# Kernel optimization log

Hardware: AMD Instinct MI355X
Metric: run time of the kernel (lower is better)

Reference implementation:

```python
import jax, jax.numpy as jnp
import numpy as np

# static config (matches init_kwargs / source constants)
B, S, CCH, NF, T = 64, 50, 3, 129, 29   # batch, seq, channels, freq bins (nfft/2+1), frames
M_FB = 32                                # filterbank size M in F1
D = 16                                   # latents -> SPD matrix size
M_OFF = D * (D - 1) // 2                 # strictly-lower Cholesky entries
HID = D + M_OFF                          # ODE state size
ODE_U = 256                              # n_units
NCLS = 5
K_EULER, DT = 4, 0.25                    # fixed-step Euler ODE solve per interval
BN_EPS = 1e-5


def lin_tri_filter(nfilt=M_FB, nfft=256, samplerate=100):
    # faithful port of FilterbankShape.lin_tri_filter_shape
    highfreq = samplerate / 2
    hz = np.linspace(0, highfreq, nfilt + 2)
    b = np.floor((nfft + 1) * hz / samplerate)
    fb = np.zeros([nfilt, nfft // 2 + 1])
    for j in range(nfilt):
        for i in range(int(b[j]), int(b[j + 1])):
            fb[j, i] = (i - b[j]) / (b[j + 1] - b[j])
        for i in range(int(b[j + 1]), int(b[j + 2])):
            fb[j, i] = (b[j + 2] - i) / (b[j + 2] - b[j + 1])
    return fb.T.astype(np.float32)  # (129, 32)


def setup_inputs() -> dict:
    key = jax.random.key(0)
    ks = jax.random.split(key, 32)
    f32 = jnp.float32
    CIN = CCH * M_FB  # 96

    def unif(k, shape, bound):
        return jax.random.uniform(k, shape, f32, -bound, bound)

    sd = 1.0 / np.sqrt(D)
    so = 1.0 / np.sqrt(M_OFF)
    cb1 = 1.0 / np.sqrt(CIN * 5)
    cb2 = 1.0 / np.sqrt(CIN * 5)
    lb = lambda fan_in: 1.0 / np.sqrt(fan_in)

    inp = {
        "x": jax.random.normal(ks[0], (B, S, CCH, NF, T), f32),
        "fw": jax.nn.sigmoid(jax.random.normal(ks[1], (NF, M_FB), f32)),
        "s_tri": jnp.asarray(lin_tri_filter()),
        "conv1_w": unif(ks[2], (CIN, CIN, 5), cb1),
        "conv1_b": unif(ks[3], (CIN,), cb1),
        "bn1_g": jnp.ones((CIN,), f32),
        "bn1_b": jnp.zeros((CIN,), f32),
        "conv2_w": unif(ks[4], (D, CIN, 5), cb2),
        "conv2_b": unif(ks[5], (D,), cb2),
        "bn2_g": jnp.ones((D,), f32),
        "bn2_b": jnp.zeros((D,), f32),
        "wx_d": unif(ks[6], (D, 3 * D), sd),
        "wh_d": unif(ks[7], (D, 3 * D), sd),
        "bias_d": unif(ks[8], (3 * D,), sd),
        "wx_o": unif(ks[9], (M_OFF, 3 * M_OFF), so),
        "wh_o": unif(ks[10], (M_OFF, 3 * M_OFF), so),
        "bias_o": unif(ks[11], (3 * M_OFF,), so),
        "ode_w0": unif(ks[12], (HID, ODE_U), lb(HID)),
        "ode_b0": unif(ks[13], (ODE_U,), lb(HID)),
        "ode_w1": unif(ks[14], (ODE_U, ODE_U), lb(ODE_U)),
        "ode_b1": unif(ks[15], (ODE_U,), lb(ODE_U)),
        "ode_w2": unif(ks[16], (ODE_U, ODE_U), lb(ODE_U)),
        "ode_b2": unif(ks[17], (ODE_U,), lb(ODE_U)),
        "ode_w3": unif(ks[18], (ODE_U, HID), lb(ODE_U)),
        "ode_b3": unif(ks[19], (HID,), lb(ODE_U)),
        "cls_w": unif(ks[20], (HID, NCLS), lb(HID)),
        "cls_b": unif(ks[21], (NCLS,), lb(HID)),
    }
    return inp


def _forward(x, fw, s_tri, conv1_w, conv1_b, bn1_g, bn1_b, conv2_w, conv2_b,
             bn2_g, bn2_b, wx_d, wh_d, bias_d, wx_o, wh_o, bias_o,
             ode_w0, ode_b0, ode_w1, ode_b1, ode_w2, ode_b2, ode_w3, ode_b3,
             cls_w, cls_b):
    b, s = x.shape[:2]
    # --- filter_bank: (b,s,C,F,T) x (F,M) -> (b,s,C*M,T) ---
    xf = jnp.einsum('bscft,fm->bscmt', x, fw * s_tri)
    h = xf.reshape(b * s, CCH * M_FB, T)
    dn = ('NCH', 'OIH', 'NCH')

    def conv_bn_lrelu(h, w, bias, g, be):
        h = jax.lax.conv_general_dilated(h, w, (1,), 'VALID', dimension_numbers=dn)
        h = h + bias[None, :, None]
        mu = h.mean((0, 2), keepdims=True)           # BatchNorm1d (train-mode stats)
        var = h.var((0, 2), keepdims=True)
        h = (h - mu) / jnp.sqrt(var + BN_EPS) * g[None, :, None] + be[None, :, None]
        return jnp.where(h >= 0, h, 0.01 * h)        # LeakyReLU

    h = conv_bn_lrelu(h, conv1_w, conv1_b, bn1_g, bn1_b)   # (bs, 96, 25)
    h = conv_bn_lrelu(h, conv2_w, conv2_b, bn2_g, bn2_b)   # (bs, D, 21)
    feats = h.transpose(0, 2, 1)                           # (bs, t, D)

    def oas(X):  # OAS-shrunk covariance, X: (n, d)
        n, d = X.shape
        xm = X - X.mean(0)
        emp = xm.T @ xm / (n - 1)
        mu = jnp.trace(emp) / d
        alpha = jnp.mean(emp ** 2)
        num = alpha + mu ** 2
        den = (n + 1.0) * (alpha - mu ** 2 / d)
        shr = jnp.where(den == 0, 1.0, jnp.minimum(num / den, 1.0))
        return (1.0 - shr) * emp + shr * mu * jnp.eye(d, dtype=X.dtype)

    covs = jax.vmap(oas)(feats)                            # (bs, D, D)
    L = jnp.linalg.cholesky(covs).reshape(b, s, D, D)
    ir, ic = np.tril_indices(D, -1)
    x_d = jnp.diagonal(L, axis1=-2, axis2=-1)              # (b,s,D) positive
    x_o = L[..., ir, ic]                                   # (b,s,M_OFF)

    def ode_net(hh):  # odefunc: Lin, [Tanh,Lin]*2, Tanh, Lin
        hh = hh @ ode_w0 + ode_b0
        hh = jnp.tanh(hh) @ ode_w1 + ode_b1
        hh = jnp.tanh(hh) @ ode_w2 + ode_b2
        return jnp.tanh(hh) @ ode_w3 + ode_b3

    abs_bd = jnp.abs(bias_d)

    def step(carry, xt):
        hd, ho = carry
        xd, xo = xt
        # ODE evolution of hidden state in Cholesky chart (log-diag || off-diag)
        hc = jnp.concatenate([jnp.log(hd), ho], -1)
        for _ in range(K_EULER):
            hc = hc + DT * ode_net(hc)
        hd = jnp.exp(hc[:, :D])
        ho = hc[:, D:]
        # diag RGRU cell (PosLinear + softplus; log/exp products simplify)
        gx = xd @ jnp.abs(wx_d)
        gh = hd @ jnp.abs(wh_d)
        ixr, ixi, ixn = jnp.split(gx, 3, 1)
        hhr, hhi, hhn = jnp.split(gh, 3, 1)
        br, bi, bn = jnp.split(abs_bd, 3)
        r = jax.nn.sigmoid(br * ixr * hhr)
        z = jax.nn.sigmoid(bi * ixi * hhi)
        ng = jax.nn.softplus(bn * ixn * r * hhn)
        hd = hd ** z * ng ** (1.0 - z)   # geodesic GRU update on positive diag
        # off-diag RGRU cell (standard Euclidean GRU)
        gx = xo @ wx_o
        gh = ho @ wh_o
        ixr, ixi, ixn = jnp.split(gx, 3, 1)
        hhr, hhi, hhn = jnp.split(gh, 3, 1)
        br2, bi2, bn2 = jnp.split(bias_o, 3)
        r = jax.nn.sigmoid(ixr + hhr + br2)
        z = jax.nn.sigmoid(ixi + hhi + bi2)
        ng = jnp.tanh(ixn + r * hhn + bn2)
        ho = ng + z * (ho - ng)
        return (hd, ho), None

    hd0 = jnp.ones((b, D), x.dtype)
    ho0 = jnp.zeros((b, M_OFF), x.dtype)
    (hd, ho), _ = jax.lax.scan(step, (hd0, ho0),
                               (x_d.transpose(1, 0, 2), x_o.transpose(1, 0, 2)))
    feat = jnp.concatenate([jnp.log(hd), ho], -1)
    return feat @ cls_w + cls_b  # (b, NCLS)


def reference(x, fw, s_tri, conv1_w, conv1_b, bn1_g, bn1_b, conv2_w, conv2_b,
              bn2_g, bn2_b, wx_d, wh_d, bias_d, wx_o, wh_o, bias_o,
              ode_w0, ode_b0, ode_w1, ode_b1, ode_w2, ode_b2, ode_w3, ode_b3,
              cls_w, cls_b):
    return _forward(x, fw, s_tri, conv1_w, conv1_b, bn1_g, bn1_b, conv2_w,
                    conv2_b, bn2_g, bn2_b, wx_d, wh_d, bias_d, wx_o, wh_o,
                    bias_o, ode_w0, ode_b0, ode_w1, ode_b1, ode_w2, ode_b2,
                    ode_w3, ode_b3, cls_w, cls_b)
```

## Files before the change

### kernel.cpp

```cpp
#include <hip/hip_runtime.h>
#include <math.h>


#define BB 64
#define NIMG 3200

typedef _Float16 f16;
typedef _Float16 f16x8 __attribute__((ext_vector_type(8)));
typedef float f32x4 __attribute__((ext_vector_type(4)));

#define HS 164
#define GS 516

__device__ __forceinline__ float fsigm(float x) {
  return __fdividef(1.f, 1.f + __expf(-x));
}
__device__ __forceinline__ float ftanh(float x) {
  return 1.f - __fdividef(2.f, __expf(2.f * x) + 1.f);
}

#define OFF_W0  0
#define OFF_W1  20480
#define OFF_W2  53248
#define OFF_W3  86016
#define OFF_GRZ 104448
#define OFF_GNX 135168
#define OFF_GNH 143360
#define PK2_TOT 151552

__global__ __launch_bounds__(256) void k1_fb(const float* __restrict__ x,
                                             const float* __restrict__ fw,
                                             const float* __restrict__ st,
                                             float* __restrict__ h1) {
  __shared__ __align__(16) float ws[129 * 32];
  __shared__ __align__(16) float xs[129 * 32];
  const int tid = threadIdx.x;
  const int n = blockIdx.x;
  const float* xp = x + (size_t)n * 11223;

  for (int i = tid; i < 4128; i += 256) ws[i] = fw[i] * st[i];

  float acc[4][4];
#pragma unroll
  for (int i = 0; i < 4; ++i)
#pragma unroll
    for (int j = 0; j < 4; ++j) acc[i][j] = 0.f;

  const int c = tid / 64;
  const int rem = tid % 64;
  const int m0 = (rem / 8) * 4;
  const int t0 = (rem % 8) * 4;

  for (int fc = 0; fc < 3; ++fc) {
    __syncthreads();
    for (int i = tid; i < 3741; i += 256) {
      int cc = i / 1247;
      int r = i - cc * 1247;
      int f = r / 29;
      int t = r - f * 29;
      xs[(cc * 43 + f) * 32 + t] = xp[cc * 3741 + (fc * 43 + f) * 29 + t];
    }
    for (int i = tid; i < 129; i += 256) {
      xs[i * 32 + 29] = 0.f; xs[i * 32 + 30] = 0.f; xs[i * 32 + 31] = 0.f;
    }
    __syncthreads();
    if (tid < 192) {
      const float* xb = xs + (c * 43) * 32 + t0;
      const float* wb = ws + (fc * 43) * 32 + m0;
      for (int f = 0; f < 43; ++f) {
        float4 xv = *(const float4*)(xb + f * 32);
        float4 wv = *(const float4*)(wb + f * 32);
        float xa[4] = {xv.x, xv.y, xv.z, xv.w};
        float wa[4] = {wv.x, wv.y, wv.z, wv.w};
#pragma unroll
        for (int i = 0; i < 4; ++i)
#pragma unroll
          for (int j = 0; j < 4; ++j) acc[i][j] += wa[i] * xa[j];
      }
    }
  }
  if (tid < 192) {
    const int nt = (t0 == 28) ? 1 : 4;
    for (int i = 0; i < 4; ++i)
      for (int j = 0; j < nt; ++j)
        h1[(size_t)n * 2784 + (size_t)(c * 32 + m0 + i) * 29 + (t0 + j)] = acc[i][j];
  }
}

__global__ __launch_bounds__(256) void k2_conv1(const float* __restrict__ h1,
                                                const float* __restrict__ w,
                                                const float* __restrict__ bias,
                                                float* __restrict__ h2,
                                                float* __restrict__ part1) {
  __shared__ __align__(16) float ins[2 * 96 * 32];
  __shared__ __align__(16) float wls[96 * 81];
  const int tid = threadIdx.x;
  const int wg = blockIdx.x;

  for (int i = tid; i < 2 * 2784; i += 256) {
    int img = i / 2784;
    int e = i - img * 2784;
    int ci = e / 29;
    int t = e - ci * 29;
    ins[img * 3072 + ci * 32 + t] = h1[(size_t)(wg * 2 + img) * 2784 + e];
  }

  const int img = tid / 96;
  const int co = tid - img * 96;
  float acc[25];
#pragma unroll
  for (int t = 0; t < 25; ++t) acc[t] = 0.f;

  for (int cc = 0; cc < 6; ++cc) {
    __syncthreads();
    for (int i = tid; i < 7680; i += 256) {
      int cw = i / 80;
      int r = i - cw * 80;
      wls[cw * 81 + r] = w[cw * 480 + cc * 80 + r];
    }
    __syncthreads();
    if (tid < 192) {
      for (int ci = 0; ci < 16; ++ci) {
        float xv[29];
#pragma unroll
        for (int j = 0; j < 29; ++j) xv[j] = ins[img * 3072 + (cc * 16 + ci) * 32 + j];
        float wv[5];
#pragma unroll
        for (int d = 0; d < 5; ++d) wv[d] = wls[co * 81 + ci * 5 + d];
#pragma unroll
        for (int t = 0; t < 25; ++t) {
          float s = acc[t];
#pragma unroll
          for (int d = 0; d < 5; ++d) s += xv[t + d] * wv[d];
          acc[t] = s;
        }
      }
    }
  }
  if (tid < 192) {
    const int n = wg * 2 + img;
    const float bval = bias[co];
    float s1 = 0.f, s2 = 0.f;
    for (int t = 0; t < 25; ++t) {
      float v = acc[t] + bval;
      h2[(size_t)n * 2400 + co * 25 + t] = v;
      s1 += v;
      s2 += v * v;
    }
    part1[((size_t)n * 96 + co) * 2 + 0] = s1;
    part1[((size_t)n * 96 + co) * 2 + 1] = s2;
  }
}

__global__ __launch_bounds__(256) void k3_bn1(const float* __restrict__ part,
                                              const float* __restrict__ gg,
                                              const float* __restrict__ be,
                                              float* __restrict__ ab) {
  __shared__ double sd[256], sq[256];
  const int c = blockIdx.x;
  const int t = threadIdx.x;
  double s = 0.0, q = 0.0;
  for (int n = t; n < NIMG; n += 256) {
    s += (double)part[((size_t)n * 96 + c) * 2 + 0];
    q += (double)part[((size_t)n * 96 + c) * 2 + 1];
  }
  sd[t] = s; sq[t] = q;
  __syncthreads();
  for (int off = 128; off > 0; off >>= 1) {
    if (t < off) { sd[t] += sd[t + off]; sq[t] += sq[t + off]; }
    __syncthreads();
  }
  if (t == 0) {
    double mu = sd[0] / 80000.0;
    double var = sq[0] / 80000.0 - mu * mu;
    float A = (float)((double)gg[c] / sqrt(var + 1e-5));
    ab[c * 2 + 0] = A;
    ab[c * 2 + 1] = (float)((double)be[c] - mu * (double)A);
  }
}

__global__ __launch_bounds__(256) void k5_bn2(const float* __restrict__ part,
                                              const float* __restrict__ gg,
                                              const float* __restrict__ be,
                                              float* __restrict__ ab) {
  __shared__ double sd[256], sq[256];
  const int c = blockIdx.x;
  const int t = threadIdx.x;
  double s = 0.0, q = 0.0;
  for (int n = t; n < 800; n += 256) {
    s += (double)part[((size_t)n * 16 + c) * 2 + 0];
    q += (double)part[((size_t)n * 16 + c) * 2 + 1];
  }
  sd[t] = s; sq[t] = q;
  __syncthreads();
  for (int off = 128; off > 0; off >>= 1) {
    if (t < off) { sd[t] += sd[t + off]; sq[t] += sq[t + off]; }
    __syncthreads();
  }
  if (t == 0) {
    double mu = sd[0] / 67200.0;
    double var = sq[0] / 67200.0 - mu * mu;
    float A = (float)((double)gg[c] / sqrt(var + 1e-5));
    ab[c * 2 + 0] = A;
    ab[c * 2 + 1] = (float)((double)be[c] - mu * (double)A);
  }
}

__global__ __launch_bounds__(256) void k4_conv2(const float* __restrict__ h2,
                                                const float* __restrict__ w,
                                                const float* __restrict__ bias,
                                                const float* __restrict__ bn1,
                                                float* __restrict__ h3,
                                                float* __restrict__ part2) {
  __shared__ __align__(16) float ins[4 * 96 * 26];
  __shared__ __align__(16) float wls[16 * 241];
  __shared__ float A1s[96], B1s[96];
  __shared__ float red[16 * 16 * 2];
  const int tid = threadIdx.x;
  const int wg = blockIdx.x;

  if (tid < 96) {
    A1s[tid] = bn1[tid * 2 + 0];
    B1s[tid] = bn1[tid * 2 + 1];
  }
  __syncthreads();
  for (int i = tid; i < 9600; i += 256) {
    int img = i / 2400;
    int e = i - img * 2400;
    int ci = e / 25;
    int t = e - ci * 25;
    float v = h2[(size_t)(wg * 4 + img) * 2400 + e];
    v = A1s[ci] * v + B1s[ci];
    v = (v >= 0.f) ? v : 0.01f * v;
    ins[img * 2496 + ci * 26 + t] = v;
  }
  for (int i = tid; i < 4 * 96; i += 256) ins[(i / 96) * 2496 + (i % 96) * 26 + 25] = 0.f;

  const int img = tid >> 6;
  const int co = (tid >> 2) & 15;
  const int tg = tid & 3;
  const int t0s[4] = {0, 6, 11, 16};
  const int t0 = t0s[tg];
  const int tl = (tg == 0) ? 6 : 5;
  float acc[6] = {0.f, 0.f, 0.f, 0.f, 0.f, 0.f};

  for (int cc = 0; cc < 2; ++cc) {
    __syncthreads();
    for (int i = tid; i < 3840; i += 256) {
      int cw = i / 240;
      int r = i - cw * 240;
      wls[cw * 241 + r] = w[cw * 480 + cc * 240 + r];
    }
    __syncthreads();
    for (int ci = 0; ci < 48; ++ci) {
      float xv[10];
#pragma unroll
      for (int j = 0; j < 10; ++j) xv[j] = ins[img * 2496 + (cc * 48 + ci) * 26 + t0 + j];
      float wv[5];
#pragma unroll
      for (int d = 0; d < 5; ++d) wv[d] = wls[co * 241 + ci * 5 + d];
#pragma unroll
      for (int t = 0; t < 6; ++t) {
        float s = acc[t];
#pragma unroll
        for (int d = 0; d < 5; ++d) s += xv[t + d] * wv[d];
        acc[t] = s;
      }
    }
  }
  const float bval = bias[co];
  float s1 = 0.f, s2 = 0.f;
  const int n = wg * 4 + img;
  for (int t = 0; t < 6; ++t) {
    if (t < tl) {
      float v = acc[t] + bval;
      h3[(size_t)n * 336 + co * 21 + t0 + t] = v;
      s1 += v;
      s2 += v * v;
    }
  }
  red[(co * 16 + img * 4 + tg) * 2 + 0] = s1;
  red[(co * 16 + img * 4 + tg) * 2 + 1] = s2;
  __syncthreads();
  if (tid < 16) {
    float s = 0.f, q = 0.f;
    for (int k = 0; k < 16; ++k) {
      s += red[(tid * 16 + k) * 2 + 0];
      q += red[(tid * 16 + k) * 2 + 1];
    }
    part2[((size_t)wg * 16 + tid) * 2 + 0] = s;
    part2[((size_t)wg * 16 + tid) * 2 + 1] = q;
  }
}

__global__ __launch_bounds__(256) void k6_oas(const float* __restrict__ h3,
                                              const float* __restrict__ bn2,
                                              float* __restrict__ xd,
                                              float* __restrict__ xo) {
  __shared__ float X[4][21 * 17 + 3];
  __shared__ float A[4][16 * 17];
  __shared__ float mcol[4][16];
  const int tid = threadIdx.x;
  const int wid = tid >> 6;
  const int lane = tid & 63;
  const int n = blockIdx.x * 4 + wid;
  const float* hp = h3 + (size_t)n * 336;

  for (int e = lane; e < 336; e += 64) {
    int c = e / 21;
    int t = e - c * 21;
    float v = hp[e];
    v = bn2[c * 2 + 0] * v + bn2[c * 2 + 1];
    v = (v >= 0.f) ? v : 0.01f * v;
    X[wid][t * 17 + c] = v;
  }
  __syncthreads();
  if (lane < 16) {
    float s = 0.f;
    for (int t = 0; t < 21; ++t) s += X[wid][t * 17 + lane];
    mcol[wid][lane] = s * (1.f / 21.f);
  }
  __syncthreads();
  for (int e = lane; e < 336; e += 64) {
    int t = e / 16;
    int c = e - t * 16;
    X[wid][t * 17 + c] -= mcol[wid][c];
  }
  __syncthreads();

  float tr_p = 0.f, al_p = 0.f;
  float ent[3];
  int ei[3], ej[3], ne = 0;
  for (int e = lane; e < 136; e += 64) {
    int i = 0, e2 = e;
    while (e2 >= 16 - i) { e2 -= 16 - i; i++; }
    int j = i + e2;
    float s = 0.f;
    for (int t = 0; t < 21; ++t) s += X[wid][t * 17 + i] * X[wid][t * 17 + j];
    s *= (1.f / 20.f);
    ent[ne] = s; ei[ne] = i; ej[ne] = j; ne++;
    if (i == j) tr_p += s;
    al_p += s * s * ((i == j) ? 1.f : 2.f);
  }
  for (int m = 1; m < 64; m <<= 1) {
    tr_p += __shfl_xor(tr_p, m);
    al_p += __shfl_xor(al_p, m);
  }
  const float mu = tr_p * (1.f / 16.f);
  const float alpha = al_p * (1.f / 256.f);
  const float num = alpha + mu * mu;
  const float den = 22.f * (alpha - mu * mu * (1.f / 16.f));
  const float shr = (den == 0.f) ? 1.f : fminf(num / den, 1.f);
  for (int q = 0; q < ne; ++q) {
    float c = (1.f - shr) * ent[q] + ((ei[q] == ej[q]) ? shr * mu : 0.f);
    A[wid][ei[q] * 17 + ej[q]] = c;
    A[wid][ej[q] * 17 + ei[q]] = c;
  }
  __syncthreads();

  for (int k = 0; k < 16; ++k) {
    float akk = A[wid][k * 17 + k];
    __syncthreads();
    float d = sqrtf(akk);
    float rd = 1.f / d;
    if (lane == k) A[wid][k * 17 + k] = d;
    if (lane > k && lane < 16) A[wid][lane * 17 + k] *= rd;
    __syncthreads();
    if (lane > k && lane < 16) {
      float Lik = A[wid][lane * 17 + k];
      for (int j = k + 1; j <= lane; ++j) A[wid][lane * 17 + j] -= Lik * A[wid][j * 17 + k];
    }
    __syncthreads();
  }
  if (lane < 16) xd[(size_t)n * 16 + lane] = A[wid][lane * 17 + lane];
  for (int p = lane; p < 120; p += 64) {
    int i = 1, p2 = p;
    while (p2 >= i) { p2 -= i; i++; }
    xo[(size_t)n * 120 + p] = A[wid][i * 17 + p2];
  }
}

__global__ __launch_bounds__(256) void k0_pack(const float* __restrict__ w0,
                                               const float* __restrict__ w1,
                                               const float* __restrict__ w2,
                                               const float* __restrict__ w3,
                                               const float* __restrict__ wxo,
                                               const float* __restrict__ who,
                                               uint32_t* __restrict__ dst) {
  int i = blockIdx.x * 256 + threadIdx.x;
  if (i >= PK2_TOT) return;
  int j = i, kind, NT;
  if (j < OFF_W1)       { kind = 0; NT = 16; }
  else if (j < OFF_W2)  { kind = 1; NT = 16; j -= OFF_W1; }
  else if (j < OFF_W3)  { kind = 2; NT = 16; j -= OFF_W2; }
  else if (j < OFF_GRZ) { kind = 3; NT = 9;  j -= OFF_W3; }
  else if (j < OFF_GNX) { kind = 4; NT = 15; j -= OFF_GRZ; }
  else if (j < OFF_GNH) { kind = 5; NT = 8;  j -= OFF_GNX; }
  else                  { kind = 6; NT = 8;  j -= OFF_GNH; }
  const int tile = j >> 8;
  const int rem = j & 255;
  const int l = rem >> 2;
  const int wd = rem & 3;
  const int t = tile / NT;
  const int nt = tile - t * NT;
  const int col = nt * 16 + (l & 15);
  const int kk = t * 32 + 8 * (l >> 4) + 2 * wd;

  float v[2];
#pragma unroll
  for (int q = 0; q < 2; ++q) {
    const int k = kk + q;
    float s = 0.f;
    if (kind == 0)      { if (k < 136) s = w0[k * 256 + col]; }
    else if (kind == 1) { s = w1[k * 256 + col]; }
    else if (kind == 2) { s = w2[k * 256 + col]; }
    else if (kind == 3) { if (col < 136) s = w3[k * 136 + col]; }
    else if (kind == 4) {
      if (k < 120) s = wxo[k * 360 + col];
      else if (k >= 128 && k < 248) s = who[(k - 128) * 360 + col];
    } else if (kind == 5) { if (k < 120 && col < 120) s = wxo[k * 360 + 240 + col]; }
    else                  { if (k < 120 && col < 120) s = who[k * 360 + 240 + col]; }
    v[q] = s;
  }
  union { f16 h[2]; uint32_t u; } cv;
  cv.h[0] = (f16)v[0];
  cv.h[1] = (f16)v[1];
  dst[i] = cv.u;
}

__device__ __forceinline__ uint4 aread_lin(const f16* X, int t, int l) {
  return ((const uint4*)X)[t * 64 + l];
}
__device__ __forceinline__ void xwrite_frag(f16* X, int row, int col, float v) {
  const int slot = row + 16 * ((col >> 3) & 3);
  const int byte = (((col >> 5) * 64 + slot) << 4) + 2 * (col & 7);
  *(f16*)((char*)X + byte) = (f16)v;
}

union UF { uint4 u; f16x8 h; };

template <int KT, int NT, int MODE>
__device__ __forceinline__ void mlp_one(const f16* __restrict__ Xin,
                                        const uint4* __restrict__ B,
                                        const float* __restrict__ bias,
                                        f16* __restrict__ Xout,
                                        float* __restrict__ hcf,
                                        f16* __restrict__ Xnext,
                                        float* __restrict__ ehl,
                                        int nt, int l) {
  if (nt < 0 || nt >= NT) return;
  const int m = l & 15;
  const int g = l >> 4;
  uint4 bf[KT];
#pragma unroll
  for (int t = 0; t < KT; ++t) bf[t] = B[(t * NT + nt) * 64 + l];
  f32x4 acc = {0.f, 0.f, 0.f, 0.f};
#pragma unroll
  for (int t = 0; t < KT; ++t) {
    UF a; a.u = aread_lin(Xin, t, l);
    UF b; b.u = bf[t];
    acc = __builtin_amdgcn_mfma_f32_16x16x32_f16(a.h, b.h, acc, 0, 0, 0);
  }
  const int col = nt * 16 + m;
  if (MODE == 0) {
    const float bb = bias[col];
#pragma unroll
    for (int i2 = 0; i2 < 4; ++i2)
      xwrite_frag(Xout, 4 * g + i2, col, ftanh(acc[i2] + bb));
  } else {
    if (col < 136) {
      const float bb = bias[col];
#pragma unroll
      for (int i2 = 0; i2 < 4; ++i2) {
        const int row = 4 * g + i2;
        float v = hcf[row * HS + col] + 0.25f * (acc[i2] + bb);
        hcf[row * HS + col] = v;
        if (MODE == 1) {
          xwrite_frag(Xnext, row, col, v);
        } else {
          if (col >= 16) xwrite_frag(Xnext, row, col + 112, v);
          else ehl[row * 16 + col] = __expf(v);
        }
      }
    }
  }
}

template <int KT, int NT>
__device__ __forceinline__ void gate_tile(const f16* __restrict__ Xin,
                                          const uint4* __restrict__ B,
                                          float* __restrict__ GO,
                                          int nt, int ktoff, int gooff, int l) {
  if (nt < 0) return;
  const int m = l & 15;
  const int g = l >> 4;
  uint4 bf[KT];
#pragma unroll
  for (int t = 0; t < KT; ++t) bf[t] = B[(t * NT + nt) * 64 + l];
  f32x4 acc = {0.f, 0.f, 0.f, 0.f};
#pragma unroll
  for (int t = 0; t < KT; ++t) {
    UF a; a.u = aread_lin(Xin, t + ktoff, l);
    UF b; b.u = bf[t];
    acc = __builtin_amdgcn_mfma_f32_16x16x32_f16(a.h, b.h, acc, 0, 0, 0);
  }
  const int col = nt * 16 + m;
#pragma unroll
  for (int i2 = 0; i2 < 4; ++i2)
    GO[(4 * g + i2) * GS + gooff + col] = acc[i2];
}

__global__ __launch_bounds__(1024, 1) void k7_scan(
    const float* __restrict__ xdv, const float* __restrict__ xov,
    const float* __restrict__ wxd, const float* __restrict__ whd,
    const float* __restrict__ bdv, const float* __restrict__ bov,
    const uint32_t* __restrict__ pk,
    const float* __restrict__ b0, const float* __restrict__ b1,
    const float* __restrict__ b2, const float* __restrict__ b3,
    const float* __restrict__ cw, const float* __restrict__ cbv,
    float* __restrict__ out) {
  __shared__ __align__(16) f16 XA[16 * 256];
  __shared__ __align__(16) f16 XB[16 * 256];
  __shared__ __align__(16) f16 XC[16 * 256];
  __shared__ __align__(16) f16 XG[16 * 256];
  __shared__ __align__(16) float GO[16 * GS];
  __shared__ __align__(16) float hcf[16 * HS];
  __shared__ __align__(16) float xdlv[16 * 16];
  __shared__ __align__(16) float ehl[16 * 16];
  __shared__ __align__(16) float G2[16 * 96];
  __shared__ __align__(16) float wdaT[48 * 16], whaT[48 * 16];
  __shared__ float b0l[256], b1l[256], b2l[256], b3l[144], bovl[360], bdvl[48];

  const int tid = threadIdx.x;
  const int w = tid >> 6;
  const int l = tid & 63;
  const int blk = blockIdx.x;

  const uint4* BW0 = (const uint4*)(pk + OFF_W0);
  const uint4* BW1 = (const uint4*)(pk + OFF_W1);
  const uint4* BW2 = (const uint4*)(pk + OFF_W2);
  const uint4* BW3 = (const uint4*)(pk + OFF_W3);
  const uint4* BRZ = (const uint4*)(pk + OFF_GRZ);
  const uint4* BNX = (const uint4*)(pk + OFF_GNX);
  const uint4* BNH = (const uint4*)(pk + OFF_GNH);

  for (int i = tid; i < 768; i += 1024) {
    int k = i / 48, c = i - k * 48;
    wdaT[c * 16 + k] = fabsf(wxd[i]);
    whaT[c * 16 + k] = fabsf(whd[i]);
  }
  for (int i = tid; i < 256; i += 1024) { b0l[i] = b0[i]; b1l[i] = b1[i]; b2l[i] = b2[i]; }
  if (tid < 144) b3l[tid] = (tid < 136) ? b3[tid] : 0.f;
  if (tid < 360) bovl[tid] = bov[tid];
  if (tid < 48) bdvl[tid] = fabsf(bdv[tid]);
  for (int i = tid; i < 16 * HS; i += 1024) hcf[i] = 0.f;
  for (int i = tid; i < 4096; i += 1024) { XA[i] = (f16)0.f; XG[i] = (f16)0.f; }
  __syncthreads();

#pragma unroll 1
  for (int s = 0; s < 50; ++s) {
#pragma unroll 1
    for (int e = 0; e < 4; ++e) {
      mlp_one<5, 16, 0>(XA, BW0, b0l, XB, nullptr, nullptr, nullptr, w, l);
      if (e == 0) {
        for (int i = tid; i < 1920; i += 1024) {
          int row = i / 120, c = i - row * 120;
          xwrite_frag(XG, row, c, xov[((size_t)(blk * 16 + row) * 50 + s) * 120 + c]);
        }
        if (tid < 256) {
          int row = tid >> 4, k = tid & 15;
          xdlv[tid] = xdv[((size_t)(blk * 16 + row) * 50 + s) * 16 + k];
        }
      }
      __syncthreads();
      mlp_one<8, 16, 0>(XB, BW1, b1l, XC, nullptr, nullptr, nullptr, w, l);
      __syncthreads();
      mlp_one<8, 16, 0>(XC, BW2, b2l, XB, nullptr, nullptr, nullptr, w, l);
      __syncthreads();
      if (e < 3)
        mlp_one<8, 9, 1>(XB, BW3, b3l, nullptr, hcf, XA, nullptr, w, l);
      else
        mlp_one<8, 9, 2>(XB, BW3, b3l, nullptr, hcf, XG, ehl, w, l);
      __syncthreads();
    }

    gate_tile<8, 15>(XG, BRZ, GO, (w < 15) ? w : -1, 0, 0, l);
    gate_tile<4, 8>(XG, BNX, GO, (w < 8) ? w : -1, 0, 256, l);
    gate_tile<4, 8>(XG, BNH, GO, (w >= 8) ? (w - 8) : -1, 4, 384, l);
    for (int i = tid; i < 1536; i += 1024) {
      int row = i / 96, c = i - row * 96;
      const float4* sv = (const float4*)((c < 48) ? &xdlv[row * 16] : &ehl[row * 16]);
      const float4* wv = (const float4*)((c < 48) ? &wdaT[c * 16] : &whaT[(c - 48) * 16]);
      float a = 0.f;
#pragma unroll
      for (int q = 0; q < 4; ++q) {
        float4 xq = sv[q], wq = wv[q];
        a += xq.x * wq.x + xq.y * wq.y + xq.z * wq.z + xq.w * wq.w;
      }
      G2[row * 96 + c] = a;
    }
    __syncthreads();

    for (int i = tid; i < 1920; i += 1024) {
      int row = i / 120, e2 = i - row * 120;
      float rr = fsigm(GO[row * GS + e2] + bovl[e2]);
      float zz = fsigm(GO[row * GS + 120 + e2] + bovl[120 + e2]);
      float ng = ftanh(GO[row * GS + 256 + e2] + rr * GO[row * GS + 384 + e2] + bovl[240 + e2]);
      float ho = hcf[row * HS + 16 + e2];
      float v = ng + zz * (ho - ng);
      hcf[row * HS + 16 + e2] = v;
      xwrite_frag(XA, row, 16 + e2, v);
    }
    if (tid < 256) {
      int row = tid >> 4, t = tid & 15;
      float ixr = G2[row * 96 + t], ixi = G2[row * 96 + 16 + t], ixn = G2[row * 96 + 32 + t];
      float hhr = G2[row * 96 + 48 + t], hhi = G2[row * 96 + 64 + t], hhn = G2[row * 96 + 80 + t];
      float br = bdvl[t], bi = bdvl[16 + t], bn = bdvl[32 + t];
      float rr = fsigm(br * ixr * hhr);
      float zz = fsigm(bi * ixi * hhi);
      float sp = bn * ixn * rr * hhn;
      float ng = (sp > 20.f) ? sp : __logf(1.f + __expf(sp));
      float ldp = hcf[row * HS + t];
      float v = zz * ldp + (1.f - zz) * __logf(ng);
      hcf[row * HS + t] = v;
      xwrite_frag(XA, row, t, v);
    }
    __syncthreads();
  }

  if (tid < 80) {
    int row = tid / 5, c = tid - row * 5;
    float a = cbv[c];
    for (int k = 0; k < 136; ++k) a += hcf[row * HS + k] * cw[k * 5 + c];
    out[(size_t)(blk * 16 + row) * 5 + c] = a;
  }
}

extern "C" void kernel_launch(void* const* d_in, const int* in_sizes, int n_in,
                              void* d_out, int out_size, void* d_ws, size_t ws_size,
                              hipStream_t stream) {
  const float* x       = (const float*)d_in[0];
  const float* fw      = (const float*)d_in[1];
  const float* s_tri   = (const float*)d_in[2];
  const float* conv1_w = (const float*)d_in[3];
  const float* conv1_b = (const float*)d_in[4];
  const float* bn1_g   = (const float*)d_in[5];
  const float* bn1_b   = (const float*)d_in[6];
  const float* conv2_w = (const float*)d_in[7];
  const float* conv2_b = (const float*)d_in[8];
  const float* bn2_g   = (const float*)d_in[9];
  const float* bn2_b   = (const float*)d_in[10];
  const float* wx_d    = (const float*)d_in[11];
  const float* wh_d    = (const float*)d_in[12];
  const float* bias_d  = (const float*)d_in[13];
  const float* wx_o    = (const float*)d_in[14];
  const float* wh_o    = (const float*)d_in[15];
  const float* bias_o  = (const float*)d_in[16];
  const float* ode_w0  = (const float*)d_in[17];
  const float* ode_b0  = (const float*)d_in[18];
  const float* ode_w1  = (const float*)d_in[19];
  const float* ode_b1  = (const float*)d_in[20];
  const float* ode_w2  = (const float*)d_in[21];
  const float* ode_b2  = (const float*)d_in[22];
  const float* ode_w3  = (const float*)d_in[23];
  const float* ode_b3  = (const float*)d_in[24];
  const float* cls_w   = (const float*)d_in[25];
  const float* cls_b   = (const float*)d_in[26];

  float* ws = (float*)d_ws;
  float* h1  = ws;
  float* h3  = ws;
  float* xd  = ws + 1075200;
  float* xo  = ws + 1126400;
  float* h2  = ws + 8908800;
  float* p1  = ws + 16588800;
  float* bn1 = ws + 17203200;
  float* p2  = ws + 17203392;
  float* bn2 = ws + 17228992;
  uint32_t* pk = (uint32_t*)(ws + 8908800);

  hipLaunchKernelGGL(k1_fb,   dim3(NIMG),   dim3(256), 0, stream, x, fw, s_tri, h1);
  hipLaunchKernelGGL(k2_conv1,dim3(NIMG/2), dim3(256), 0, stream, h1, conv1_w, conv1_b, h2, p1);
  hipLaunchKernelGGL(k3_bn1,  dim3(96),     dim3(256), 0, stream, p1, bn1_g, bn1_b, bn1);
  hipLaunchKernelGGL(k4_conv2,dim3(NIMG/4), dim3(256), 0, stream, h2, conv2_w, conv2_b, bn1, h3, p2);
  hipLaunchKernelGGL(k5_bn2,  dim3(16),     dim3(256), 0, stream, p2, bn2_g, bn2_b, bn2);
  hipLaunchKernelGGL(k6_oas,  dim3(NIMG/4), dim3(256), 0, stream, h3, bn2, xd, xo);
  hipLaunchKernelGGL(k0_pack, dim3((PK2_TOT + 255) / 256), dim3(256), 0, stream,
                     ode_w0, ode_w1, ode_w2, ode_w3, wx_o, wh_o, pk);
  hipLaunchKernelGGL(k7_scan, dim3(4),      dim3(1024), 0, stream,
                     xd, xo, wx_d, wh_d, bias_d, bias_o, pk,
                     ode_b0, ode_b1, ode_b2, ode_b3, cls_w, cls_b, (float*)d_out);
}
```

Measured before the change: 1.874 ms.

## Prefetch next layer's MFMA weight fragments during current layer's matmul

Replaces the per-layer weight-fragment loads in the ODE MLP and the r/z gate tile with a register buffer. Each layer loads the next stage's B fragments (next MLP layer, the r/z gate weights, or layer 0 of the next Euler step) inside its MFMA loop. The goal is to hide global/L2 load latency behind compute and barriers in this sequential, latency-bound scan. In exchange it holds more registers live, adds branchy per-wave selection logic, and ties each wave's buffer contents to the order of stages.

Result: no change. 1.868 ms (-0.3%).

```diff
diff --git a/kernel.cpp b/kernel.cpp
--- a/kernel.cpp
+++ b/kernel.cpp
@@ -440,27 +440,30 @@
 union UF { uint4 u; f16x8 h; };
 
 template <int KT, int NT, int MODE>
-__device__ __forceinline__ void mlp_one(const f16* __restrict__ Xin,
-                                        const uint4* __restrict__ B,
-                                        const float* __restrict__ bias,
-                                        f16* __restrict__ Xout,
-                                        float* __restrict__ hcf,
-                                        f16* __restrict__ Xnext,
-                                        float* __restrict__ ehl,
-                                        int nt, int l) {
-  if (nt < 0 || nt >= NT) return;
+__device__ __forceinline__ void mlp_pf(const f16* __restrict__ Xin,
+                                       const float* __restrict__ bias,
+                                       f16* __restrict__ Xout,
+                                       float* __restrict__ hcf,
+                                       f16* __restrict__ Xnext,
+                                       float* __restrict__ ehl,
+                                       int nt, int l,
+                                       uint4 (&bf)[8],
+                                       const uint4* __restrict__ B2,
+                                       int NT2, int nt2, int nkt2) {
   const int m = l & 15;
   const int g = l >> 4;
-  uint4 bf[KT];
-#pragma unroll
-  for (int t = 0; t < KT; ++t) bf[t] = B[(t * NT + nt) * 64 + l];
+  const bool act = (nt >= 0 && nt < NT);
   f32x4 acc = {0.f, 0.f, 0.f, 0.f};
 #pragma unroll
-  for (int t = 0; t < KT; ++t) {
-    UF a; a.u = aread_lin(Xin, t, l);
-    UF b; b.u = bf[t];
-    acc = __builtin_amdgcn_mfma_f32_16x16x32_f16(a.h, b.h, acc, 0, 0, 0);
-  }
+  for (int t = 0; t < 8; ++t) {
+    if (t < KT && act) {
+      UF a; a.u = aread_lin(Xin, t, l);
+      UF b; b.u = bf[t];
+      acc = __builtin_amdgcn_mfma_f32_16x16x32_f16(a.h, b.h, acc, 0, 0, 0);
+    }
+    if (nt2 >= 0 && t < nkt2) bf[t] = B2[(t * NT2 + nt2) * 64 + l];
+  }
+  if (!act) return;
   const int col = nt * 16 + m;
   if (MODE == 0) {
     const float bb = bias[col];
@@ -487,6 +490,27 @@
 }
 
 template <int KT, int NT>
+__device__ __forceinline__ void gate_rz(const f16* __restrict__ Xin,
+                                        float* __restrict__ GO,
+                                        int nt, int gooff, int l,
+                                        uint4 (&bf)[8]) {
+  if (nt < 0) return;
+  const int m = l & 15;
+  const int g = l >> 4;
+  f32x4 acc = {0.f, 0.f, 0.f, 0.f};
+#pragma unroll
+  for (int t = 0; t < KT; ++t) {
+    UF a; a.u = aread_lin(Xin, t, l);
+    UF b; b.u = bf[t];
+    acc = __builtin_amdgcn_mfma_f32_16x16x32_f16(a.h, b.h, acc, 0, 0, 0);
+  }
+  const int col = nt * 16 + m;
+#pragma unroll
+  for (int i2 = 0; i2 < 4; ++i2)
+    GO[(4 * g + i2) * GS + gooff + col] = acc[i2];
+}
+
+template <int KT, int NT>
 __device__ __forceinline__ void gate_tile(const f16* __restrict__ Xin,
                                           const uint4* __restrict__ B,
                                           float* __restrict__ GO,
@@ -494,14 +518,14 @@
   if (nt < 0) return;
   const int m = l & 15;
   const int g = l >> 4;
-  uint4 bf[KT];
-#pragma unroll
-  for (int t = 0; t < KT; ++t) bf[t] = B[(t * NT + nt) * 64 + l];
+  uint4 bfx[KT];
+#pragma unroll
+  for (int t = 0; t < KT; ++t) bfx[t] = B[(t * NT + nt) * 64 + l];
   f32x4 acc = {0.f, 0.f, 0.f, 0.f};
 #pragma unroll
   for (int t = 0; t < KT; ++t) {
     UF a; a.u = aread_lin(Xin, t + ktoff, l);
-    UF b; b.u = bf[t];
+    UF b; b.u = bfx[t];
     acc = __builtin_amdgcn_mfma_f32_16x16x32_f16(a.h, b.h, acc, 0, 0, 0);
   }
   const int col = nt * 16 + m;
@@ -555,13 +579,17 @@
   if (tid < 48) bdvl[tid] = fabsf(bdv[tid]);
   for (int i = tid; i < 16 * HS; i += 1024) hcf[i] = 0.f;
   for (int i = tid; i < 4096; i += 1024) { XA[i] = (f16)0.f; XG[i] = (f16)0.f; }
+
+  uint4 bf[8];
+#pragma unroll
+  for (int t = 0; t < 5; ++t) bf[t] = BW0[(t * 16 + w) * 64 + l];
   __syncthreads();
 
 #pragma unroll 1
   for (int s = 0; s < 50; ++s) {
 #pragma unroll 1
     for (int e = 0; e < 4; ++e) {
-      mlp_one<5, 16, 0>(XA, BW0, b0l, XB, nullptr, nullptr, nullptr, w, l);
+      mlp_pf<5, 16, 0>(XA, b0l, XB, nullptr, nullptr, nullptr, w, l, bf, BW1, 16, w, 8);
       if (e == 0) {
         for (int i = tid; i < 1920; i += 1024) {
           int row = i / 120, c = i - row * 120;
@@ -573,18 +601,30 @@
         }
       }
       __syncthreads();
-      mlp_one<8, 16, 0>(XB, BW1, b1l, XC, nullptr, nullptr, nullptr, w, l);
+      mlp_pf<8, 16, 0>(XB, b1l, XC, nullptr, nullptr, nullptr, w, l, bf, BW2, 16, w, 8);
       __syncthreads();
-      mlp_one<8, 16, 0>(XC, BW2, b2l, XB, nullptr, nullptr, nullptr, w, l);
+      {
+        const uint4* nb; int nNT, nnt, nk;
+        if (w < 9)       { nb = BW3; nNT = 9;  nnt = w;                  nk = 8; }
+        else if (e == 3) { nb = BRZ; nNT = 15; nnt = (w < 15) ? w : -1;  nk = 8; }
+        else             { nb = BW0; nNT = 16; nnt = w;                  nk = 5; }
+        mlp_pf<8, 16, 0>(XC, b2l, XB, nullptr, nullptr, nullptr, w, l, bf, nb, nNT, nnt, nk);
+      }
       __syncthreads();
-      if (e < 3)
-        mlp_one<8, 9, 1>(XB, BW3, b3l, nullptr, hcf, XA, nullptr, w, l);
-      else
-        mlp_one<8, 9, 2>(XB, BW3, b3l, nullptr, hcf, XG, ehl, w, l);
+      {
+        const uint4* nb = (e == 3) ? BRZ : BW0;
+        const int nNT = (e == 3) ? 15 : 16;
+        const int nnt = (w < 9) ? w : -1;
+        const int nk = (e == 3) ? 8 : 5;
+        if (e < 3)
+          mlp_pf<8, 9, 1>(XB, b3l, nullptr, hcf, XA, nullptr, (w < 9) ? w : -1, l, bf, nb, nNT, nnt, nk);
+        else
+          mlp_pf<8, 9, 2>(XB, b3l, nullptr, hcf, XG, ehl, (w < 9) ? w : -1, l, bf, nb, nNT, nnt, nk);
+      }
       __syncthreads();
     }
 
-    gate_tile<8, 15>(XG, BRZ, GO, (w < 15) ? w : -1, 0, 0, l);
+    gate_rz<8, 15>(XG, GO, (w < 15) ? w : -1, 0, l, bf);
     gate_tile<4, 8>(XG, BNX, GO, (w < 8) ? w : -1, 0, 256, l);
     gate_tile<4, 8>(XG, BNH, GO, (w >= 8) ? (w - 8) : -1, 4, 384, l);
     for (int i = tid; i < 1536; i += 1024) {
@@ -601,6 +641,8 @@
     }
     __syncthreads();
 
+#pragma unroll
+    for (int t = 0; t < 5; ++t) bf[t] = BW0[(t * 16 + w) * 64 + l];
     for (int i = tid; i < 1920; i += 1024) {
       int row = i / 120, e2 = i - row * 120;
       float rr = fsigm(GO[row * GS + e2] + bovl[e2]);
```
